# Performance work log

Measured on AMD Instinct MI355X. Metric: run time of the kernel, lower is better.

The kernel has to match this reference:

```python
import jax, jax.numpy as jnp
import numpy as np

N_NODES = 100000
N_EDGES = 6400000
N_GRAPHS = 32


def _inv_softplus(x):
    return x + np.log(-np.expm1(-x))


def setup_inputs() -> dict:
    key = jax.random.key(0)
    k1, k2, k3, k4 = jax.random.split(key, 4)
    # edge displacement vectors (bond lengths ~ O(1-4) Angstrom-ish)
    r = jax.random.normal(k1, (N_EDGES, 3), dtype=jnp.float32) * 2.0
    src = jax.random.randint(k2, (N_EDGES,), 0, N_NODES)
    dst = jax.random.randint(k3, (N_EDGES,), 0, N_NODES)
    node2graph = jnp.sort(jax.random.randint(k4, (N_NODES,), 0, N_GRAPHS))
    return {
        "r": r,
        "src": src,
        "dst": dst,
        "node2graph": node2graph,
        "raw_dens_amp": jnp.float32(_inv_softplus(3.0)),
        "raw_dens_ls": jnp.float32(_inv_softplus(1.5)),
        "raw_rep_amp": jnp.float32(_inv_softplus(10.0)),
        "raw_rep_ls": jnp.float32(_inv_softplus(5.0)),
        "raw_emb_amp": jnp.float32(_inv_softplus(3.0)),
        "num_nodes": N_NODES,
        "num_graphs": N_GRAPHS,
    }


def reference(r, src, dst, node2graph, raw_dens_amp, raw_dens_ls,
              raw_rep_amp, raw_rep_ls, raw_emb_amp, num_nodes, num_graphs):
    sp = jax.nn.softplus

    def energy(r_):
        bondlen = jnp.linalg.norm(r_, axis=1)                      # [E]
        # ExponentialDensity on each edge
        dens = sp(raw_dens_amp) * jnp.exp(-sp(raw_dens_ls) * bondlen)
        # update_all(copy_e, sum): scatter-sum edge density onto dst nodes
        local_density = jax.ops.segment_sum(dens, dst, num_segments=num_nodes)
        # SqrtEmbedding (eps-clamped so grad at exactly-zero density is finite)
        F = -sp(raw_emb_amp) * jnp.sqrt(jnp.maximum(local_density, 1e-12))
        # ExponentialRepulsive per edge
        rep = sp(raw_rep_amp) * jnp.exp(-sp(raw_rep_ls) * bondlen)
        # graph-level readouts
        e_node = jax.ops.segment_sum(F, node2graph, num_segments=num_graphs)
        e_edge = jax.ops.segment_sum(rep, node2graph[dst], num_segments=num_graphs)
        return e_node + e_edge                                     # [G]

    total_energy, pullback = jax.vjp(energy, r)
    (dE_dr,) = pullback(jnp.ones_like(total_energy))               # [E,3]
    # autograd forces: r_ij points src -> dst, so dE/dpos_dst += dE/dr,
    # dE/dpos_src -= dE/dr; force = -dE/dpos
    forces = (jax.ops.segment_sum(-dE_dr, dst, num_segments=num_nodes)
              + jax.ops.segment_sum(dE_dr, src, num_segments=num_nodes))
    return total_energy, forces
```

## Files before the change

kernel.cpp:

```cpp
#include <hip/hip_runtime.h>
#include <math.h>

#define NG 32
#define T_N 40704
#define T_C 20352

#define PK_Q   32.0f
#define PK_K1  8589934592.0
#define PK_K2  131072.0

__device__ __forceinline__ float softplus_f(float x) {
    return (x > 0.f) ? (x + log1pf(expf(-x))) : log1pf(expf(x));
}

__device__ __forceinline__ void lds_fadd64(double* p, double v) {
#if defined(__HIP_PLATFORM_AMD__) || defined(__AMDGCN__)
    unsafeAtomicAdd(p, v);
#else
    atomicAdd(p, v);
#endif
}

__device__ __forceinline__ void map_tc(int gid, int NT, int NC, int* t, int* c) {
    if ((NC & 7) == 0) {
        int x = gid & 7, s = gid >> 3;
        *t = s % NT;
        *c = (s / NT) * 8 + x;
    } else {
        *t = gid / NC;
        *c = gid - (*t) * NC;
    }
}

__global__ __launch_bounds__(256) void k1_dens(
        const float* __restrict__ r,
        const float* __restrict__ p_da, const float* __restrict__ p_dl,
        float* __restrict__ dens_arr, int E)
{
    const float Ad = softplus_f(*p_da), Ld = softplus_f(*p_dl);
    const float4* r4 = (const float4*)r;
    float4* dens4 = (float4*)dens_arr;
    const int NQ = E >> 2;
    const int stride = gridDim.x * blockDim.x;
    for (int q = blockIdx.x*blockDim.x + threadIdx.x; q < NQ; q += stride) {
        float4 a = r4[3*q], b = r4[3*q+1], c = r4[3*q+2];
        float bl0 = sqrtf(a.x*a.x + a.y*a.y + a.z*a.z);
        float bl1 = sqrtf(a.w*a.w + b.x*b.x + b.y*b.y);
        float bl2 = sqrtf(b.z*b.z + b.w*b.w + c.x*c.x);
        float bl3 = sqrtf(c.y*c.y + c.z*c.z + c.w*c.w);
        float4 dv = { Ad*expf(-Ld*bl0), Ad*expf(-Ld*bl1),
                      Ad*expf(-Ld*bl2), Ad*expf(-Ld*bl3) };
        dens4[q] = dv;
    }
    for (int e = (NQ<<2) + blockIdx.x*blockDim.x + threadIdx.x; e < E; e += stride) {
        float x = r[3*e], y = r[3*e+1], z = r[3*e+2];
        float bl = sqrtf(x*x + y*y + z*z);
        dens_arr[e] = Ad*expf(-Ld*bl);
    }
}

__global__ __launch_bounds__(512) void k2_dens_tiles(
        const float* __restrict__ dens_arr, const int* __restrict__ dst,
        float* __restrict__ scratch, int E, int NT, int NC)
{
    __shared__ float sd[T_N];
    int t, k;
    map_tc(blockIdx.x, NT, NC, &t, &k);
    const int base = t * T_N;
    for (int i = threadIdx.x; i < T_N; i += blockDim.x) sd[i] = 0.f;
    __syncthreads();
    const int NQ = E >> 2;
    const int cq = (NQ + NC - 1) / NC;
    const int q0 = k*cq;
    const int q1 = (q0 + cq < NQ) ? (q0 + cq) : NQ;
    const float4* dens4 = (const float4*)dens_arr;
    const int4*   d4 = (const int4*)dst;
    for (int q = q0 + (int)threadIdx.x; q < q1; q += (int)blockDim.x) {
        float4 dv = dens4[q]; int4 dd = d4[q];
        unsigned l;
        l = (unsigned)(dd.x - base); if (l < T_N) atomicAdd(&sd[l], dv.x);
        l = (unsigned)(dd.y - base); if (l < T_N) atomicAdd(&sd[l], dv.y);
        l = (unsigned)(dd.z - base); if (l < T_N) atomicAdd(&sd[l], dv.z);
        l = (unsigned)(dd.w - base); if (l < T_N) atomicAdd(&sd[l], dv.w);
    }
    if (k == NC-1) {
        for (int e = (NQ<<2) + (int)threadIdx.x; e < E; e += (int)blockDim.x) {
            unsigned l = (unsigned)(dst[e] - base);
            if (l < T_N) atomicAdd(&sd[l], dens_arr[e]);
        }
    }
    __syncthreads();
    size_t sb = (size_t)(t * NC + k) * T_N;
    for (int i = threadIdx.x; i < T_N; i += blockDim.x) scratch[sb + i] = sd[i];
}

__global__ __launch_bounds__(256) void k3_node(
        const float* __restrict__ scratch, const int* __restrict__ n2g,
        const float* __restrict__ p_ea,
        float* __restrict__ g_out, float* __restrict__ e_graph, int N, int NC)
{
    __shared__ float sbin[NG];
    if (threadIdx.x < NG) sbin[threadIdx.x] = 0.f;
    __syncthreads();
    const float Ae = softplus_f(*p_ea);
    int n = blockIdx.x*blockDim.x + threadIdx.x;
    if (n < N) {
        int t = n / T_N; int off = n - t*T_N;
        const float* bp = scratch + ((size_t)t*NC)*T_N + off;
        float l = 0.f;
        for (int k = 0; k < NC; ++k) l += bp[(size_t)k*T_N];
        float s = sqrtf(fmaxf(l, 1e-12f));
        atomicAdd(&sbin[n2g[n]], -Ae*s);
        g_out[n] = (l >= 1e-12f) ? (-0.5f*Ae/s) : 0.f;
    }
    __syncthreads();
    if (threadIdx.x < NG) atomicAdd(&e_graph[threadIdx.x], sbin[threadIdx.x]);
}

__global__ __launch_bounds__(256) void k4_fvec(
        const float* __restrict__ r, const int* __restrict__ dst,
        const int* __restrict__ n2g, const float* __restrict__ g,
        const float* __restrict__ p_da, const float* __restrict__ p_dl,
        const float* __restrict__ p_ra, const float* __restrict__ p_rl,
        float* __restrict__ fvec, float* __restrict__ e_graph, int E)
{
    __shared__ float sbin[NG];
    if (threadIdx.x < NG) sbin[threadIdx.x] = 0.f;
    __syncthreads();
    const float Ad = softplus_f(*p_da), Ld = softplus_f(*p_dl);
    const float Ar = softplus_f(*p_ra), Lr = softplus_f(*p_rl);
    const float4* r4 = (const float4*)r;
    const int4*   d4 = (const int4*)dst;
    float4* f4 = (float4*)fvec;
    const int NQ = E >> 2;
    const int stride = gridDim.x * blockDim.x;
    for (int q = blockIdx.x*blockDim.x + threadIdx.x; q < NQ; q += stride) {
        float4 a = r4[3*q], b = r4[3*q+1], c = r4[3*q+2];
        int4 dd = d4[q];
        float g0 = g[dd.x], g1 = g[dd.y], g2 = g[dd.z], g3 = g[dd.w];
        int b0 = n2g[dd.x], b1 = n2g[dd.y], b2 = n2g[dd.z], b3 = n2g[dd.w];
        float bl0 = sqrtf(a.x*a.x + a.y*a.y + a.z*a.z);
        float bl1 = sqrtf(a.w*a.w + b.x*b.x + b.y*b.y);
        float bl2 = sqrtf(b.z*b.z + b.w*b.w + c.x*c.x);
        float bl3 = sqrtf(c.y*c.y + c.z*c.z + c.w*c.w);
        float rep0 = Ar*expf(-Lr*bl0), rep1 = Ar*expf(-Lr*bl1);
        float rep2 = Ar*expf(-Lr*bl2), rep3 = Ar*expf(-Lr*bl3);
        float de0 = g0*(-Ld*Ad*expf(-Ld*bl0)) - Lr*rep0;
        float de1 = g1*(-Ld*Ad*expf(-Ld*bl1)) - Lr*rep1;
        float de2 = g2*(-Ld*Ad*expf(-Ld*bl2)) - Lr*rep2;
        float de3 = g3*(-Ld*Ad*expf(-Ld*bl3)) - Lr*rep3;
        float s0 = (bl0 > 0.f) ? de0/bl0 : 0.f;
        float s1 = (bl1 > 0.f) ? de1/bl1 : 0.f;
        float s2 = (bl2 > 0.f) ? de2/bl2 : 0.f;
        float s3 = (bl3 > 0.f) ? de3/bl3 : 0.f;
        float4 o0 = { s0*a.x, s0*a.y, s0*a.z, s1*a.w };
        float4 o1 = { s1*b.x, s1*b.y, s2*b.z, s2*b.w };
        float4 o2 = { s2*c.x, s3*c.y, s3*c.z, s3*c.w };
        f4[3*q] = o0; f4[3*q+1] = o1; f4[3*q+2] = o2;
        atomicAdd(&sbin[b0], rep0);
        atomicAdd(&sbin[b1], rep1);
        atomicAdd(&sbin[b2], rep2);
        atomicAdd(&sbin[b3], rep3);
    }
    for (int e = (NQ<<2) + blockIdx.x*blockDim.x + threadIdx.x; e < E; e += stride) {
        float x = r[3*e], y = r[3*e+1], z = r[3*e+2];
        float bl = sqrtf(x*x + y*y + z*z);
        int de = dst[e];
        float rep = Ar*expf(-Lr*bl);
        float dEdb = g[de]*(-Ld*Ad*expf(-Ld*bl)) - Lr*rep;
        float s = (bl > 0.f) ? dEdb/bl : 0.f;
        fvec[3*e] = s*x; fvec[3*e+1] = s*y; fvec[3*e+2] = s*z;
        atomicAdd(&sbin[n2g[de]], rep);
    }
    __syncthreads();
    if (threadIdx.x < NG) atomicAdd(&e_graph[threadIdx.x], sbin[threadIdx.x]);
}

__device__ __forceinline__ double pk3(float fx, float fy, float fz) {
    double hx = (double)rintf(fx * PK_Q);
    double hy = (double)rintf(fy * PK_Q);
    return hx * PK_K1 + hy * PK_K2 + (double)fz;
}

__device__ __forceinline__ void fscat64(double* sf, int base, int d, int s, double p) {
    unsigned ld = (unsigned)(d - base);
    if (ld < T_C) lds_fadd64(&sf[ld], -p);
    unsigned ls = (unsigned)(s - base);
    if (ls < T_C) lds_fadd64(&sf[ls],  p);
}

__global__ __launch_bounds__(512) void k5_pk64(
        const float* __restrict__ fvec, const int* __restrict__ src,
        const int* __restrict__ dst,
        double* __restrict__ scratch, int E, int NT, int NC)
{
    __shared__ double sf[T_C];
    int t, c;
    map_tc(blockIdx.x, NT, NC, &t, &c);
    const int base = t * T_C;
    for (int i = threadIdx.x; i < T_C; i += blockDim.x) sf[i] = 0.0;
    __syncthreads();
    const int NQ = E >> 2;
    const int cq = (NQ + NC - 1) / NC;
    const int q0 = c*cq;
    const int q1 = (q0 + cq < NQ) ? (q0 + cq) : NQ;
    const float4* f4 = (const float4*)fvec;
    const int4* d4 = (const int4*)dst;
    const int4* s4 = (const int4*)src;
    for (int q = q0 + (int)threadIdx.x; q < q1; q += (int)blockDim.x) {
        float4 a = f4[3*q], b = f4[3*q+1], cc = f4[3*q+2];
        int4 dd = d4[q]; int4 ss = s4[q];
        double p0 = pk3(a.x,  a.y,  a.z);
        double p1 = pk3(a.w,  b.x,  b.y);
        double p2 = pk3(b.z,  b.w,  cc.x);
        double p3 = pk3(cc.y, cc.z, cc.w);
        fscat64(sf, base, dd.x, ss.x, p0);
        fscat64(sf, base, dd.y, ss.y, p1);
        fscat64(sf, base, dd.z, ss.z, p2);
        fscat64(sf, base, dd.w, ss.w, p3);
    }
    if (c == NC-1) {
        for (int e = (NQ<<2) + (int)threadIdx.x; e < E; e += (int)blockDim.x) {
            double p = pk3(fvec[3*e], fvec[3*e+1], fvec[3*e+2]);
            fscat64(sf, base, dst[e], src[e], p);
        }
    }
    __syncthreads();
    size_t sb = (size_t)(t * NC + c) * T_C;
    for (int i = threadIdx.x; i < T_C; i += blockDim.x) scratch[sb + i] = sf[i];
}

__global__ __launch_bounds__(256) void k6_pk64(
        const double* __restrict__ scratch, float* __restrict__ forces,
        int N, int NC)
{
    int n = blockIdx.x*blockDim.x + threadIdx.x;
    if (n >= N) return;
    int t = n / T_C; int off = n - t*T_C;
    const double* bp = scratch + ((size_t)t*NC)*T_C + off;
    double V = 0.0;
    for (int k = 0; k < NC; ++k) V += bp[(size_t)k*T_C];
    double h1 = rint(V * (1.0/PK_K1));
    double rem = V - h1 * PK_K1;
    double h2 = rint(rem * (1.0/PK_K2));
    double Z = rem - h2 * PK_K2;
    forces[3*n+0] = (float)(h1 * (1.0/(double)PK_Q));
    forces[3*n+1] = (float)(h2 * (1.0/(double)PK_Q));
    forces[3*n+2] = (float)Z;
}


__global__ __launch_bounds__(256) void fb_pass1(
        const float* __restrict__ r, const int* __restrict__ dst,
        const int* __restrict__ n2g,
        const float* __restrict__ p_da, const float* __restrict__ p_dl,
        const float* __restrict__ p_ra, const float* __restrict__ p_rl,
        float* __restrict__ local_density, float* __restrict__ e_graph, int E)
{
    __shared__ float sbin[NG];
    if (threadIdx.x < NG) sbin[threadIdx.x] = 0.f;
    __syncthreads();
    const float Ad = softplus_f(*p_da), Ld = softplus_f(*p_dl);
    const float Ar = softplus_f(*p_ra), Lr = softplus_f(*p_rl);
    const int stride = gridDim.x * blockDim.x;
    for (int e = blockIdx.x*blockDim.x + threadIdx.x; e < E; e += stride) {
        float x = r[3*e], y = r[3*e+1], z = r[3*e+2];
        float bl = sqrtf(x*x + y*y + z*z);
        int de = dst[e];
        atomicAdd(&local_density[de], Ad*expf(-Ld*bl));
        atomicAdd(&sbin[n2g[de]], Ar*expf(-Lr*bl));
    }
    __syncthreads();
    if (threadIdx.x < NG) atomicAdd(&e_graph[threadIdx.x], sbin[threadIdx.x]);
}

__global__ __launch_bounds__(256) void fb_pass2(
        float* __restrict__ ld_g, const int* __restrict__ n2g,
        const float* __restrict__ p_ea, float* __restrict__ e_graph, int N)
{
    __shared__ float sbin[NG];
    if (threadIdx.x < NG) sbin[threadIdx.x] = 0.f;
    __syncthreads();
    const float Ae = softplus_f(*p_ea);
    const int stride = gridDim.x * blockDim.x;
    for (int n = blockIdx.x*blockDim.x + threadIdx.x; n < N; n += stride) {
        float l = ld_g[n];
        float s = sqrtf(fmaxf(l, 1e-12f));
        atomicAdd(&sbin[n2g[n]], -Ae*s);
        ld_g[n] = (l >= 1e-12f) ? (-0.5f*Ae/s) : 0.f;
    }
    __syncthreads();
    if (threadIdx.x < NG) atomicAdd(&e_graph[threadIdx.x], sbin[threadIdx.x]);
}

__global__ __launch_bounds__(256) void fb_pass3(
        const float* __restrict__ r, const int* __restrict__ src,
        const int* __restrict__ dst, const float* __restrict__ g,
        const float* __restrict__ p_da, const float* __restrict__ p_dl,
        const float* __restrict__ p_ra, const float* __restrict__ p_rl,
        float* __restrict__ forces, int E)
{
    const float Ad = softplus_f(*p_da), Ld = softplus_f(*p_dl);
    const float Ar = softplus_f(*p_ra), Lr = softplus_f(*p_rl);
    const int stride = gridDim.x * blockDim.x;
    for (int e = blockIdx.x*blockDim.x + threadIdx.x; e < E; e += stride) {
        float x = r[3*e], y = r[3*e+1], z = r[3*e+2];
        float bl = sqrtf(x*x + y*y + z*z);
        int de = dst[e], se = src[e];
        float dEdb = g[de]*(-Ld*Ad*expf(-Ld*bl)) - Lr*Ar*expf(-Lr*bl);
        float s = (bl > 0.f) ? dEdb/bl : 0.f;
        float fx = s*x, fy = s*y, fz = s*z;
        atomicAdd(&forces[3*de+0], -fx); atomicAdd(&forces[3*de+1], -fy); atomicAdd(&forces[3*de+2], -fz);
        atomicAdd(&forces[3*se+0],  fx); atomicAdd(&forces[3*se+1],  fy); atomicAdd(&forces[3*se+2],  fz);
    }
}

extern "C" void kernel_launch(void* const* d_in, const int* in_sizes, int n_in,
                              void* d_out, int out_size, void* d_ws, size_t ws_size,
                              hipStream_t stream) {
    const float* r    = (const float*)d_in[0];
    const int*   src  = (const int*)d_in[1];
    const int*   dst  = (const int*)d_in[2];
    const int*   n2g  = (const int*)d_in[3];
    const float* p_da = (const float*)d_in[4];
    const float* p_dl = (const float*)d_in[5];
    const float* p_ra = (const float*)d_in[6];
    const float* p_rl = (const float*)d_in[7];
    const float* p_ea = (const float*)d_in[8];

    const int E = in_sizes[1];
    const int N = in_sizes[3];

    float* e_graph = (float*)d_out;
    float* forces  = (float*)d_out + NG;

    const int E4 = (E + 3) & ~3;
    const int NT_D = (N + T_N - 1) / T_N;
    const int NT_C = (N + T_C - 1) / T_C;

    const size_t wsf_n    = ws_size / 4;
    const size_t n_ld     = ((size_t)N + 63) & ~(size_t)63;
    const size_t off_edge = n_ld;
    const size_t off_scr  = (off_edge + (size_t)3 * (size_t)E4 + 1) & ~(size_t)1;

    long avail = (long)wsf_n - (long)off_scr;
    int NC_D = 0, NC_F = 0;
    if (avail > 0) {
        long cd = avail / ((long)NT_D * T_N);
        long cf = avail / ((long)NT_C * T_C * 2);
        NC_D = (int)(cd > 80 ? 80 : cd);
        NC_F = (int)(cf > 48 ? 48 : cf);
        if (NC_D >= 8) NC_D &= ~7;
        if (NC_F >= 8) NC_F &= ~7;
    }

    const int NQ = E >> 2;
    int ge = (NQ + 255) / 256; if (ge > 2048) ge = 2048;

    if (NC_D >= 1 && NC_F >= 1) {
        float*  ld_g     = (float*)d_ws;
        float*  edgebuf  = (float*)d_ws + off_edge;
        float*  scratchf = (float*)d_ws + off_scr;
        double* scratchd = (double*)scratchf;

        hipMemsetAsync(d_out, 0, NG * sizeof(float), stream);

        k1_dens<<<ge, 256, 0, stream>>>(r, p_da, p_dl, edgebuf, E);
        k2_dens_tiles<<<NT_D * NC_D, 512, 0, stream>>>(edgebuf, dst, scratchf,
                                                       E, NT_D, NC_D);
        k3_node<<<(N + 255) / 256, 256, 0, stream>>>(scratchf, n2g, p_ea,
                                                     ld_g, e_graph, N, NC_D);
        k4_fvec<<<ge, 256, 0, stream>>>(r, dst, n2g, ld_g, p_da, p_dl, p_ra, p_rl,
                                        edgebuf, e_graph, E);
        k5_pk64<<<NT_C * NC_F, 512, 0, stream>>>(edgebuf, src, dst,
                                                 scratchd, E, NT_C, NC_F);
        k6_pk64<<<(N + 255) / 256, 256, 0, stream>>>(scratchd, forces, N, NC_F);
    } else {
        float* ld_g = (float*)d_ws;
        hipMemsetAsync(d_out, 0, (size_t)out_size * sizeof(float), stream);
        hipMemsetAsync(d_ws, 0, (size_t)N * sizeof(float), stream);
        int geb = (E + 255) / 256; if (geb > 2048) geb = 2048;
        fb_pass1<<<geb, 256, 0, stream>>>(r, dst, n2g, p_da, p_dl, p_ra, p_rl,
                                          ld_g, e_graph, E);
        fb_pass2<<<(N + 255) / 256, 256, 0, stream>>>(ld_g, n2g, p_ea, e_graph, N);
        fb_pass3<<<geb, 256, 0, stream>>>(r, src, dst, ld_g, p_da, p_dl, p_ra, p_rl,
                                          forces, E);
    }
}
```

Baseline: 237.4 us.

## Pack force vectors to doubles in k4 and replace n2g gather with boundary search

The edge kernel now writes each edge's force vector already packed into one double (8 bytes instead of 12), so the scatter kernel reads less data and skips the packing arithmetic. A new small kernel computes graph boundary offsets from the sorted node2graph array, and the edge kernel finds each edge's graph with a binary search over those boundaries in shared memory instead of a random global gather. The per-block repulsion bins are replicated four ways to reduce LDS atomic contention. Correctness relies on node2graph being sorted, and the workspace layout is changed to fit the boundary array.

```diff
diff --git a/kernel.cpp b/kernel.cpp
--- a/kernel.cpp
+++ b/kernel.cpp
@@ -30,6 +30,17 @@
         *t = gid / NC;
         *c = gid - (*t) * NC;
     }
+}
+
+__global__ __launch_bounds__(256) void k0_bounds(
+        const int* __restrict__ n2g, int* __restrict__ B, int N)
+{
+    int n = blockIdx.x*blockDim.x + threadIdx.x;
+    if (n >= N) return;
+    int v = n2g[n];
+    int p = (n == 0) ? -1 : n2g[n-1];
+    for (int g = p+1; g <= v; ++g) B[g] = n;
+    if (n == N-1) for (int g = v+1; g <= NG; ++g) B[g] = N;
 }
 
 __global__ __launch_bounds__(256) void k1_dens(
@@ -117,28 +128,46 @@
     if (threadIdx.x < NG) atomicAdd(&e_graph[threadIdx.x], sbin[threadIdx.x]);
 }
 
-__global__ __launch_bounds__(256) void k4_fvec(
+__device__ __forceinline__ double pk3(float fx, float fy, float fz) {
+    double hx = (double)rintf(fx * PK_Q);
+    double hy = (double)rintf(fy * PK_Q);
+    return hx * PK_K1 + hy * PK_K2 + (double)fz;
+}
+
+__device__ __forceinline__ int gid_of(const int* sB, int x) {
+    int lo = 0;
+    lo += (sB[lo+16] <= x) ? 16 : 0;
+    lo += (sB[lo+8]  <= x) ? 8  : 0;
+    lo += (sB[lo+4]  <= x) ? 4  : 0;
+    lo += (sB[lo+2]  <= x) ? 2  : 0;
+    lo += (sB[lo+1]  <= x) ? 1  : 0;
+    return lo;
+}
+
+__global__ __launch_bounds__(256) void k4_pd(
         const float* __restrict__ r, const int* __restrict__ dst,
-        const int* __restrict__ n2g, const float* __restrict__ g,
+        const int* __restrict__ B, const float* __restrict__ g,
         const float* __restrict__ p_da, const float* __restrict__ p_dl,
         const float* __restrict__ p_ra, const float* __restrict__ p_rl,
-        float* __restrict__ fvec, float* __restrict__ e_graph, int E)
-{
-    __shared__ float sbin[NG];
-    if (threadIdx.x < NG) sbin[threadIdx.x] = 0.f;
+        double* __restrict__ pd, float* __restrict__ e_graph, int E)
+{
+    __shared__ float sbin[NG*4];
+    __shared__ int sB[NG+2];
+    if (threadIdx.x < NG*4) sbin[threadIdx.x] = 0.f;
+    if (threadIdx.x < NG+1) sB[threadIdx.x] = B[threadIdx.x];
+    if (threadIdx.x == 0) sB[NG+1] = 0x7fffffff;
     __syncthreads();
     const float Ad = softplus_f(*p_da), Ld = softplus_f(*p_dl);
     const float Ar = softplus_f(*p_ra), Lr = softplus_f(*p_rl);
     const float4* r4 = (const float4*)r;
     const int4*   d4 = (const int4*)dst;
-    float4* f4 = (float4*)fvec;
     const int NQ = E >> 2;
     const int stride = gridDim.x * blockDim.x;
+    const int rep_slot = ((int)threadIdx.x & 3) << 5;
     for (int q = blockIdx.x*blockDim.x + threadIdx.x; q < NQ; q += stride) {
         float4 a = r4[3*q], b = r4[3*q+1], c = r4[3*q+2];
         int4 dd = d4[q];
         float g0 = g[dd.x], g1 = g[dd.y], g2 = g[dd.z], g3 = g[dd.w];
-        int b0 = n2g[dd.x], b1 = n2g[dd.y], b2 = n2g[dd.z], b3 = n2g[dd.w];
         float bl0 = sqrtf(a.x*a.x + a.y*a.y + a.z*a.z);
         float bl1 = sqrtf(a.w*a.w + b.x*b.x + b.y*b.y);
         float bl2 = sqrtf(b.z*b.z + b.w*b.w + c.x*c.x);
@@ -153,14 +182,14 @@
         float s1 = (bl1 > 0.f) ? de1/bl1 : 0.f;
         float s2 = (bl2 > 0.f) ? de2/bl2 : 0.f;
         float s3 = (bl3 > 0.f) ? de3/bl3 : 0.f;
-        float4 o0 = { s0*a.x, s0*a.y, s0*a.z, s1*a.w };
-        float4 o1 = { s1*b.x, s1*b.y, s2*b.z, s2*b.w };
-        float4 o2 = { s2*c.x, s3*c.y, s3*c.z, s3*c.w };
-        f4[3*q] = o0; f4[3*q+1] = o1; f4[3*q+2] = o2;
-        atomicAdd(&sbin[b0], rep0);
-        atomicAdd(&sbin[b1], rep1);
-        atomicAdd(&sbin[b2], rep2);
-        atomicAdd(&sbin[b3], rep3);
+        pd[4*q+0] = pk3(s0*a.x, s0*a.y, s0*a.z);
+        pd[4*q+1] = pk3(s1*a.w, s1*b.x, s1*b.y);
+        pd[4*q+2] = pk3(s2*b.z, s2*b.w, s2*c.x);
+        pd[4*q+3] = pk3(s3*c.y, s3*c.z, s3*c.w);
+        atomicAdd(&sbin[gid_of(sB, dd.x) + rep_slot], rep0);
+        atomicAdd(&sbin[gid_of(sB, dd.y) + rep_slot], rep1);
+        atomicAdd(&sbin[gid_of(sB, dd.z) + rep_slot], rep2);
+        atomicAdd(&sbin[gid_of(sB, dd.w) + rep_slot], rep3);
     }
     for (int e = (NQ<<2) + blockIdx.x*blockDim.x + threadIdx.x; e < E; e += stride) {
         float x = r[3*e], y = r[3*e+1], z = r[3*e+2];
@@ -169,17 +198,11 @@
         float rep = Ar*expf(-Lr*bl);
         float dEdb = g[de]*(-Ld*Ad*expf(-Ld*bl)) - Lr*rep;
         float s = (bl > 0.f) ? dEdb/bl : 0.f;
-        fvec[3*e] = s*x; fvec[3*e+1] = s*y; fvec[3*e+2] = s*z;
-        atomicAdd(&sbin[n2g[de]], rep);
-    }
-    __syncthreads();
-    if (threadIdx.x < NG) atomicAdd(&e_graph[threadIdx.x], sbin[threadIdx.x]);
-}
-
-__device__ __forceinline__ double pk3(float fx, float fy, float fz) {
-    double hx = (double)rintf(fx * PK_Q);
-    double hy = (double)rintf(fy * PK_Q);
-    return hx * PK_K1 + hy * PK_K2 + (double)fz;
+        pd[e] = pk3(s*x, s*y, s*z);
+        atomicAdd(&sbin[gid_of(sB, de) + rep_slot], rep);
+    }
+    __syncthreads();
+    if (threadIdx.x < NG*4) atomicAdd(&e_graph[threadIdx.x & (NG-1)], sbin[threadIdx.x]);
 }
 
 __device__ __forceinline__ void fscat64(double* sf, int base, int d, int s, double p) {
@@ -190,7 +213,7 @@
 }
 
 __global__ __launch_bounds__(512) void k5_pk64(
-        const float* __restrict__ fvec, const int* __restrict__ src,
+        const double* __restrict__ pd, const int* __restrict__ src,
         const int* __restrict__ dst,
         double* __restrict__ scratch, int E, int NT, int NC)
 {
@@ -204,25 +227,20 @@
     const int cq = (NQ + NC - 1) / NC;
     const int q0 = c*cq;
     const int q1 = (q0 + cq < NQ) ? (q0 + cq) : NQ;
-    const float4* f4 = (const float4*)fvec;
+    const double2* pd2 = (const double2*)pd;
     const int4* d4 = (const int4*)dst;
     const int4* s4 = (const int4*)src;
     for (int q = q0 + (int)threadIdx.x; q < q1; q += (int)blockDim.x) {
-        float4 a = f4[3*q], b = f4[3*q+1], cc = f4[3*q+2];
+        double2 pa = pd2[2*q], pb = pd2[2*q+1];
         int4 dd = d4[q]; int4 ss = s4[q];
-        double p0 = pk3(a.x,  a.y,  a.z);
-        double p1 = pk3(a.w,  b.x,  b.y);
-        double p2 = pk3(b.z,  b.w,  cc.x);
-        double p3 = pk3(cc.y, cc.z, cc.w);
-        fscat64(sf, base, dd.x, ss.x, p0);
-        fscat64(sf, base, dd.y, ss.y, p1);
-        fscat64(sf, base, dd.z, ss.z, p2);
-        fscat64(sf, base, dd.w, ss.w, p3);
+        fscat64(sf, base, dd.x, ss.x, pa.x);
+        fscat64(sf, base, dd.y, ss.y, pa.y);
+        fscat64(sf, base, dd.z, ss.z, pb.x);
+        fscat64(sf, base, dd.w, ss.w, pb.y);
     }
     if (c == NC-1) {
         for (int e = (NQ<<2) + (int)threadIdx.x; e < E; e += (int)blockDim.x) {
-            double p = pk3(fvec[3*e], fvec[3*e+1], fvec[3*e+2]);
-            fscat64(sf, base, dst[e], src[e], p);
+            fscat64(sf, base, dst[e], src[e], pd[e]);
         }
     }
     __syncthreads();
@@ -340,8 +358,9 @@
 
     const size_t wsf_n    = ws_size / 4;
     const size_t n_ld     = ((size_t)N + 63) & ~(size_t)63;
-    const size_t off_edge = n_ld;
-    const size_t off_scr  = (off_edge + (size_t)3 * (size_t)E4 + 1) & ~(size_t)1;
+    const size_t off_B    = n_ld;
+    const size_t off_edge = n_ld + 64;
+    const size_t off_scr  = off_edge + (size_t)2 * (size_t)E4;
 
     long avail = (long)wsf_n - (long)off_scr;
     int NC_D = 0, NC_F = 0;
@@ -359,20 +378,23 @@
 
     if (NC_D >= 1 && NC_F >= 1) {
         float*  ld_g     = (float*)d_ws;
+        int*    Bptr     = (int*)((float*)d_ws + off_B);
         float*  edgebuf  = (float*)d_ws + off_edge;
+        double* pd       = (double*)edgebuf;
         float*  scratchf = (float*)d_ws + off_scr;
         double* scratchd = (double*)scratchf;
 
         hipMemsetAsync(d_out, 0, NG * sizeof(float), stream);
 
+        k0_bounds<<<(N + 255) / 256, 256, 0, stream>>>(n2g, Bptr, N);
         k1_dens<<<ge, 256, 0, stream>>>(r, p_da, p_dl, edgebuf, E);
         k2_dens_tiles<<<NT_D * NC_D, 512, 0, stream>>>(edgebuf, dst, scratchf,
                                                        E, NT_D, NC_D);
         k3_node<<<(N + 255) / 256, 256, 0, stream>>>(scratchf, n2g, p_ea,
                                                      ld_g, e_graph, N, NC_D);
-        k4_fvec<<<ge, 256, 0, stream>>>(r, dst, n2g, ld_g, p_da, p_dl, p_ra, p_rl,
-                                        edgebuf, e_graph, E);
-        k5_pk64<<<NT_C * NC_F, 512, 0, stream>>>(edgebuf, src, dst,
+        k4_pd<<<ge, 256, 0, stream>>>(r, dst, Bptr, ld_g, p_da, p_dl, p_ra, p_rl,
+                                      pd, e_graph, E);
+        k5_pk64<<<NT_C * NC_F, 512, 0, stream>>>(pd, src, dst,
                                                  scratchd, E, NT_C, NC_F);
         k6_pk64<<<(N + 255) / 256, 256, 0, stream>>>(scratchd, forces, N, NC_F);
     } else {
```

Result: slower. 450.1 us (+89.6%).
